# Performance work log

Hardware: AMD Instinct MI355X
Metric: run time of the kernel (lower is better)

Reference implementation:

```python
import jax, jax.numpy as jnp
import numpy as np
from bisect import bisect

# hyperparameters (from init_kwargs)
DELTA = 1e-4
GAMMA = 0.1
UTILITY_SCALE = -0.01
PRIORITY_RAIL = 0.5
LOSS_BALANCE = 1.0
ALPHA_ELU = 1.0
ENTROPY_THRESHOLDS = [0, 10, 50]
ENTROPY_LEVELS = [0.0, 0.05, 0.1, 1.0]
MASK_LEVEL = 10000.0

N = 512


def setup_inputs() -> dict:
    key = jax.random.key(0)
    k1, k2, k3, k4 = jax.random.split(key, 4)
    soft_adj = jax.random.uniform(k1, (N, N), dtype=jnp.float32)
    # original adjacency is a binary {0,1} float mask
    original_adj = (jax.random.uniform(k2, (N, N)) > 0.5).astype(jnp.float32)
    distances = jax.random.uniform(k3, (N, N), dtype=jnp.float32) * 100.0
    flow = jax.random.uniform(k4, (N, N), dtype=jnp.float32) * 10.0
    epoch = 20  # python int, selects entropy penalty level via bisect
    return {"soft_adj": soft_adj, "original_adj": original_adj,
            "distances": distances, "flow": flow, "epoch": epoch}


def _shortest_path(soft_adj, distances):
    """Soft (softmin via logsumexp) Floyd-Warshall all-pairs shortest path."""
    W = distances / (soft_adj + DELTA)          # [N, N] effective edge weights
    n = W.shape[0]
    w0 = W * (1.0 - jnp.eye(n, dtype=W.dtype))  # zero diagonal

    def step(w, k):
        # softmin(w, w[:,k,None] + w[None,k,:]) without materializing a stack
        path_through_k = w[:, k][:, None] + w[k, :][None, :]
        w_new = -GAMMA * jnp.logaddexp(-w / GAMMA, -path_through_k / GAMMA)
        return w_new, None

    w_dist, _ = jax.lax.scan(step, w0, jnp.arange(n))
    return w_dist


def reference(soft_adj, original_adj, distances, flow, epoch):
    loss_cost = jnp.sum(soft_adj * distances)

    shortest_paths = _shortest_path(soft_adj, distances)

    exp_ut_rail = jnp.exp(UTILITY_SCALE * shortest_paths * PRIORITY_RAIL)
    exp_ut_base = jnp.exp(UTILITY_SCALE * distances)
    choice_matrix = exp_ut_rail / (exp_ut_rail + exp_ut_base)
    distance_saved = distances - PRIORITY_RAIL * shortest_paths
    utility_gain = flow * choice_matrix * distance_saved
    utility_gain = jax.nn.elu(utility_gain, alpha=ALPHA_ELU) + ALPHA_ELU

    inverse_soft = jnp.eye(soft_adj.shape[0], dtype=soft_adj.dtype) - soft_adj
    entropy_loss = jnp.sum(jnp.square(soft_adj * inverse_soft))
    entropy_scale = ENTROPY_LEVELS[bisect(ENTROPY_THRESHOLDS, epoch)]

    mask_loss = jnp.sum(soft_adj * (1.0 - original_adj))

    return (loss_cost
            + LOSS_BALANCE * jnp.sum(utility_gain)
            + entropy_loss * entropy_scale
            + MASK_LEVEL * mask_loss)
```

## Files before the change

kernel.cpp:

```cpp
#include <hip/hip_runtime.h>
#include <math.h>

#define NN 512
#define KP 64
#define NPANEL 8
#define NTHR 256
#define NBLK 256
#define TRUNITS (448 * 112)

#define D_   0
#define V_   4160
#define B2_  8320
#define UB_  12672
#define SB_  17024
#define H_   21376
#define LDSN 25728

__device__ __forceinline__ float einit(const float* s, const float* dI, int i, int j) {
  float w = dI[i * NN + j] / (s[i * NN + j] + 1e-4f);
  if (i == j) w = 0.f;
  return expf(-10.f * w);
}

__global__ __launch_bounds__(NTHR) void fw_phase(
    const float* __restrict__ s, const float* __restrict__ dI,
    float* __restrict__ E, float* __restrict__ Cs, float* __restrict__ Rs,
    float* __restrict__ out, int p) {
  __shared__ __align__(16) float lds[LDSN];
  const int blk = blockIdx.x, tid = threadIdx.x;
  const int k0 = p * KP;

  if (blk >= 32) {
    const int gt = (blk - 32) * NTHR + tid;
    if (p == 0) {
      if (blk == 32 && tid == 0) out[0] = 0.f;
      if (gt < TRUNITS) {
        const int ii = gt / 112;
        const int jj = gt - ii * 112;
        const int i = ii + KP;
        const int j = (jj + 16) << 2;
        const int idx = i * NN + j;
        const float4 sv = *(const float4*)(s + idx);
        const float4 dv = *(const float4*)(dI + idx);
        float w0 = dv.x / (sv.x + 1e-4f); if (i == j + 0) w0 = 0.f;
        float w1 = dv.y / (sv.y + 1e-4f); if (i == j + 1) w1 = 0.f;
        float w2 = dv.z / (sv.z + 1e-4f); if (i == j + 2) w2 = 0.f;
        float w3 = dv.w / (sv.w + 1e-4f); if (i == j + 3) w3 = 0.f;
        *(float4*)(E + idx) = make_float4(expf(-10.f * w0), expf(-10.f * w1),
                                          expf(-10.f * w2), expf(-10.f * w3));
      }
    } else if (gt < TRUNITS) {
      const int ii = gt / 112;
      const int jj = gt - ii * 112;
      const int i = (ii < k0) ? ii : ii + KP;
      const int j = ((jj < (p << 4)) ? jj : jj + 16) << 2;
      const int idx = i * NN + j;
      const float* Cprev = Cs + (size_t)(p - 1) * (NN * KP);
      const float* Rprev = Rs + (size_t)(p - 1) * (KP * NN);
      float4 acc = *(const float4*)(E + idx);
      const float* crow = Cprev + (size_t)i * KP;
      const float* rcol = Rprev + j;
#pragma unroll 8
      for (int r = 0; r < KP; ++r) {
        const float cv = crow[r];
        const float4 rv = *(const float4*)(rcol + (size_t)r * NN);
        acc.x += cv * rv.x; acc.y += cv * rv.y;
        acc.z += cv * rv.z; acc.w += cv * rv.w;
      }
      *(float4*)(E + idx) = acc;
    }
    return;
  }

  const bool isC = (blk < 16);
  const int sb = (blk >> 1) & 7;
  const int h = blk & 1;
  const int sOff = sb * KP;
  const bool haveSl = (sb != p);
  const float* Cprev = Cs + (size_t)(p - 1) * (NN * KP);
  const float* Rprev = Rs + (size_t)(p - 1) * (KP * NN);

  if (p == 0) {
    for (int e = tid; e < 4096; e += NTHR) {
      const int a = e >> 6, b = e & 63;
      const float v = einit(s, dI, a, b);
      lds[D_ + a * 65 + b] = v;
      if (blk == 0) E[a * NN + b] = v;
    }
    if (haveSl) {
      if (isC) {
        for (int e = tid; e < 2048; e += NTHR) {
          const int a = 32 * h + (e >> 6), b = e & 63;
          const float v = einit(s, dI, sOff + a, b);
          lds[V_ + a * 65 + b] = v;
          E[(sOff + a) * NN + b] = v;
        }
      } else {
        for (int e = tid; e < 2048; e += NTHR) {
          const int m = e >> 5, j = 32 * h + (e & 31);
          const float v = einit(s, dI, m, sOff + j);
          lds[V_ + j * 65 + m] = v;
          E[m * NN + (sOff + j)] = v;
        }
      }
    }
  } else {
#pragma unroll
    for (int k = 0; k < 4; ++k) {
      const int e4 = tid + k * NTHR;
      const int a = e4 >> 4, b4 = (e4 & 15) << 2;
      *(float4*)&lds[B2_ + a * 68 + b4] =
          *(const float4*)(Cprev + (size_t)(k0 + a) * KP + b4);
      *(float4*)&lds[UB_ + a * 68 + b4] =
          *(const float4*)(Rprev + (size_t)a * NN + (k0 + b4));
      if (haveSl) {
        if (isC)
          *(float4*)&lds[SB_ + a * 68 + b4] =
              *(const float4*)(Cprev + (size_t)(sOff + a) * KP + b4);
        else
          *(float4*)&lds[SB_ + a * 68 + b4] =
              *(const float4*)(Rprev + (size_t)a * NN + (sOff + b4));
      }
    }
    __syncthreads();
    {
      const int r0 = (tid >> 4) << 2, m0 = (tid & 15) << 2;
      float acc[4][4];
#pragma unroll
      for (int i2 = 0; i2 < 4; ++i2) {
        const float4 ev = *(const float4*)(E + (size_t)(k0 + r0 + i2) * NN + (k0 + m0));
        acc[i2][0] = ev.x; acc[i2][1] = ev.y; acc[i2][2] = ev.z; acc[i2][3] = ev.w;
      }
      for (int rr = 0; rr < KP; ++rr) {
        const float4 b4 = *(const float4*)&lds[UB_ + rr * 68 + m0];
#pragma unroll
        for (int i2 = 0; i2 < 4; ++i2) {
          const float av = lds[B2_ + (r0 + i2) * 68 + rr];
          acc[i2][0] += av * b4.x; acc[i2][1] += av * b4.y;
          acc[i2][2] += av * b4.z; acc[i2][3] += av * b4.w;
        }
      }
#pragma unroll
      for (int i2 = 0; i2 < 4; ++i2)
#pragma unroll
        for (int j2 = 0; j2 < 4; ++j2)
          lds[D_ + (r0 + i2) * 65 + (m0 + j2)] = acc[i2][j2];
    }
  }
  __syncthreads();

  if (tid < 64) {
    float x[64];
    if (isC) {
#pragma unroll
      for (int a = 0; a < 64; ++a) x[a] = lds[D_ + a * 65 + tid];
    } else {
#pragma unroll
      for (int a = 0; a < 64; ++a) x[a] = lds[D_ + tid * 65 + a];
    }
#pragma unroll
    for (int m = 0; m < 64; ++m) {
      const float xm = x[m];
      lds[H_ + m * 68 + tid] = xm;
#pragma unroll
      for (int a = 0; a < 64; ++a) {
        const int sa = __builtin_amdgcn_readlane(__float_as_int(x[a]), m);
        x[a] += __int_as_float(sa) * xm;
      }
    }
  } else if (tid < 192) {
    const int tt = tid - 64;
    if (haveSl && p > 0) {
      float acc[4][4];
      if (isC) {
        const int r0 = 32 * h + ((tt >> 4) << 2);
        const int m0 = (tt & 15) << 2;
#pragma unroll
        for (int i2 = 0; i2 < 4; ++i2) {
          const float4 ev = *(const float4*)(E + (size_t)(sOff + r0 + i2) * NN + (k0 + m0));
          acc[i2][0] = ev.x; acc[i2][1] = ev.y; acc[i2][2] = ev.z; acc[i2][3] = ev.w;
        }
        for (int rr = 0; rr < KP; ++rr) {
          const float4 b4 = *(const float4*)&lds[UB_ + rr * 68 + m0];
#pragma unroll
          for (int i2 = 0; i2 < 4; ++i2) {
            const float av = lds[SB_ + (r0 + i2) * 68 + rr];
            acc[i2][0] += av * b4.x; acc[i2][1] += av * b4.y;
            acc[i2][2] += av * b4.z; acc[i2][3] += av * b4.w;
          }
        }
#pragma unroll
        for (int i2 = 0; i2 < 4; ++i2) {
          *(float4*)(E + (size_t)(sOff + r0 + i2) * NN + (k0 + m0)) =
              make_float4(acc[i2][0], acc[i2][1], acc[i2][2], acc[i2][3]);
#pragma unroll
          for (int j2 = 0; j2 < 4; ++j2)
            lds[V_ + (r0 + i2) * 65 + (m0 + j2)] = acc[i2][j2];
        }
      } else {
        const int r0 = (tt & 15) << 2;
        const int c0 = 32 * h + ((tt >> 4) << 2);
#pragma unroll
        for (int i2 = 0; i2 < 4; ++i2) {
          const float4 ev = *(const float4*)(E + (size_t)(k0 + r0 + i2) * NN + (sOff + c0));
          acc[i2][0] = ev.x; acc[i2][1] = ev.y; acc[i2][2] = ev.z; acc[i2][3] = ev.w;
        }
        for (int rr = 0; rr < KP; ++rr) {
          const float4 b4 = *(const float4*)&lds[SB_ + rr * 68 + c0];
#pragma unroll
          for (int i2 = 0; i2 < 4; ++i2) {
            const float av = lds[B2_ + (r0 + i2) * 68 + rr];
            acc[i2][0] += av * b4.x; acc[i2][1] += av * b4.y;
            acc[i2][2] += av * b4.z; acc[i2][3] += av * b4.w;
          }
        }
#pragma unroll
        for (int i2 = 0; i2 < 4; ++i2) {
          *(float4*)(E + (size_t)(k0 + r0 + i2) * NN + (sOff + c0)) =
              make_float4(acc[i2][0], acc[i2][1], acc[i2][2], acc[i2][3]);
#pragma unroll
          for (int j2 = 0; j2 < 4; ++j2)
            lds[V_ + (c0 + j2) * 65 + (r0 + i2)] = acc[i2][j2];
        }
      }
    } else if (!haveSl) {
      for (int e = tt; e < 4096; e += 128) {
        const int a = e >> 6, b = e & 63;
        lds[V_ + a * 65 + b] = isC ? lds[D_ + a * 65 + b] : lds[D_ + b * 65 + a];
      }
    }
  }
  __syncthreads();

  for (int cch = 0; cch < 4; ++cch) {
    const int mb = cch * 16;
    if (cch > 0 && tid < 128) {
      const int r = 32 * h + (tid & 31);
      const int g = tid >> 5;
      const int m0c = mb + 4 * g;
      const int vb = V_ + r * 65;
      float a0 = lds[vb + m0c + 0], a1 = lds[vb + m0c + 1];
      float a2 = lds[vb + m0c + 2], a3 = lds[vb + m0c + 3];
      for (int mp = 0; mp < mb; ++mp) {
        const float vr = lds[vb + mp];
        const float4 u4 = *(const float4*)&lds[H_ + mp * 68 + m0c];
        a0 += vr * u4.x; a1 += vr * u4.y; a2 += vr * u4.z; a3 += vr * u4.w;
      }
      lds[vb + m0c + 0] = a0; lds[vb + m0c + 1] = a1;
      lds[vb + m0c + 2] = a2; lds[vb + m0c + 3] = a3;
    }
    __syncthreads();
    if (tid < 32) {
      const int r = 32 * h + tid;
      const int vb = V_ + r * 65 + mb;
      float v[16];
#pragma unroll
      for (int u2 = 0; u2 < 16; ++u2) v[u2] = lds[vb + u2];
#pragma unroll
      for (int mp = 0; mp < 15; ++mp) {
        const float vmp = v[mp];
#pragma unroll
        for (int m2 = mp + 1; m2 < 16; ++m2)
          v[m2] += vmp * lds[H_ + (mb + mp) * 68 + (mb + m2)];
      }
#pragma unroll
      for (int u2 = 0; u2 < 16; ++u2) lds[vb + u2] = v[u2];
    }
    __syncthreads();
  }

  float* Cp = Cs + (size_t)p * (NN * KP);
  float* Rp = Rs + (size_t)p * (KP * NN);
  if (isC) {
    for (int e = tid; e < 2048; e += NTHR) {
      const int a = 32 * h + (e >> 6), b = e & 63;
      Cp[(size_t)(sOff + a) * KP + b] = lds[V_ + a * 65 + b];
    }
  } else {
    for (int e = tid; e < 2048; e += NTHR) {
      const int m = e >> 5, j = 32 * h + (e & 31);
      Rp[(size_t)m * NN + (sOff + j)] = lds[V_ + j * 65 + m];
    }
  }
}

__device__ __forceinline__ float loss_elem(float Ev, float sv, float ov,
                                           float dv, float fv, int i, int j,
                                           float esc) {
  const float sp = (Ev > 0.f) ? (-0.1f * logf(Ev)) : 1e9f;
  const float ur = expf(-0.005f * sp);
  const float ub = expf(-0.01f * dv);
  const float choice = ur / (ur + ub);
  const float ug = fv * choice * (dv - 0.5f * sp);
  const float util = (ug > 0.f) ? (ug + 1.f) : expf(ug);
  const float ent = sv * (((i == j) ? 1.f : 0.f) - sv);
  return sv * dv + util + esc * ent * ent + 10000.f * (sv * (1.f - ov));
}

__global__ __launch_bounds__(NTHR) void k_loss(
    const float* __restrict__ s, const float* __restrict__ o,
    const float* __restrict__ dI, const float* __restrict__ f,
    const int* __restrict__ ep, const float* __restrict__ E,
    const float* __restrict__ Cs, const float* __restrict__ Rs,
    float* __restrict__ out) {
  __shared__ float red[NTHR];
  const int tid = threadIdx.x;
  const int g = blockIdx.x * NTHR + tid;
  const int idx0 = g * 4;
  const int i = idx0 >> 9;
  const int j = idx0 & (NN - 1);
  const float* C7 = Cs + (size_t)7 * (NN * KP);
  const float* R7 = Rs + (size_t)7 * (KP * NN);
  float4 acc = *(const float4*)(E + idx0);
  {
    const float* crow = C7 + (size_t)i * KP;
    const float* rcol = R7 + j;
#pragma unroll 8
    for (int r = 0; r < KP; ++r) {
      const float cv = crow[r];
      const float4 rv = *(const float4*)(rcol + (size_t)r * NN);
      acc.x += cv * rv.x; acc.y += cv * rv.y;
      acc.z += cv * rv.z; acc.w += cv * rv.w;
    }
  }
  const int bi = i >> 6, bj = j >> 6;
  if (bi == bj && bi >= 1) {
    const float* cf = Cs + (size_t)(bi - 1) * (NN * KP) + (size_t)i * KP;
    const float* rf = Rs + (size_t)(bi - 1) * (KP * NN) + j;
#pragma unroll 8
    for (int r = 0; r < KP; ++r) {
      const float cv = cf[r];
      const float4 rv = *(const float4*)(rf + (size_t)r * NN);
      acc.x += cv * rv.x; acc.y += cv * rv.y;
      acc.z += cv * rv.z; acc.w += cv * rv.w;
    }
  }
  const float4 sv = *(const float4*)(s + idx0);
  const float4 ov = *(const float4*)(o + idx0);
  const float4 dv = *(const float4*)(dI + idx0);
  const float4 fv = *(const float4*)(f + idx0);
  const int e = ep[0];
  const float esc = (e < 0) ? 0.f : (e < 10) ? 0.05f : (e < 50) ? 0.1f : 1.f;
  float lsum = loss_elem(acc.x, sv.x, ov.x, dv.x, fv.x, i, j + 0, esc)
             + loss_elem(acc.y, sv.y, ov.y, dv.y, fv.y, i, j + 1, esc)
             + loss_elem(acc.z, sv.z, ov.z, dv.z, fv.z, i, j + 2, esc)
             + loss_elem(acc.w, sv.w, ov.w, dv.w, fv.w, i, j + 3, esc);
  red[tid] = lsum;
  __syncthreads();
#pragma unroll
  for (int st = 128; st > 0; st >>= 1) {
    if (tid < st) red[tid] += red[tid + st];
    __syncthreads();
  }
  if (tid == 0) atomicAdd(out, red[0]);
}

extern "C" void kernel_launch(void* const* d_in, const int* in_sizes, int n_in,
                              void* d_out, int out_size, void* d_ws, size_t ws_size,
                              hipStream_t stream) {
  const float* s = (const float*)d_in[0];
  const float* o = (const float*)d_in[1];
  const float* d = (const float*)d_in[2];
  const float* f = (const float*)d_in[3];
  const int* ep = (const int*)d_in[4];

  float* E = (float*)d_ws;
  float* Cs = E + NN * NN;
  float* Rs = Cs + NPANEL * NN * KP;
  float* out = (float*)d_out;

  for (int p = 0; p < NPANEL; ++p)
    fw_phase<<<NBLK, NTHR, 0, stream>>>(s, d, E, Cs, Rs, out, p);
  k_loss<<<NBLK, NTHR, 0, stream>>>(s, o, d, f, ep, E, Cs, Rs, out);
}
```

Measured before the change: 244.3 us.

## Overlap panel evolution with triangular solve chunks and vectorize LDS GEMM loads

```diff
diff --git a/kernel.cpp b/kernel.cpp
--- a/kernel.cpp
+++ b/kernel.cpp
@@ -20,6 +20,55 @@
   float w = dI[i * NN + j] / (s[i * NN + j] + 1e-4f);
   if (i == j) w = 0.f;
   return expf(-10.f * w);
+}
+
+template <int M0, int M1>
+__device__ __forceinline__ void evolve_seg(float* lds, float (&x)[64], int tid) {
+#pragma unroll
+  for (int m = M0; m < M1; ++m) {
+    const float xm = x[m];
+    lds[H_ + m * 68 + tid] = xm;
+#pragma unroll
+    for (int a = m + 1; a < 64; ++a) {
+      const int sa = __builtin_amdgcn_readlane(__float_as_int(x[a]), m);
+      x[a] += __int_as_float(sa) * xm;
+    }
+  }
+}
+
+__device__ __forceinline__ void pgemm_chunk(float* lds, int cch, int tt2, int h) {
+  const int mb = cch * 16;
+  const int r = 32 * h + (tt2 & 31);
+  const int g = tt2 >> 5;
+  const int m0c = mb + 4 * g;
+  const int vb = V_ + r * 65;
+  float a0 = lds[vb + m0c + 0], a1 = lds[vb + m0c + 1];
+  float a2 = lds[vb + m0c + 2], a3 = lds[vb + m0c + 3];
+  for (int mp = 0; mp < mb; ++mp) {
+    const float vr = lds[vb + mp];
+    const float4 u4 = *(const float4*)&lds[H_ + mp * 68 + m0c];
+    a0 += vr * u4.x; a1 += vr * u4.y; a2 += vr * u4.z; a3 += vr * u4.w;
+  }
+  lds[vb + m0c + 0] = a0; lds[vb + m0c + 1] = a1;
+  lds[vb + m0c + 2] = a2; lds[vb + m0c + 3] = a3;
+}
+
+__device__ __forceinline__ void micro_chunk(float* lds, int cch, int t3, int h) {
+  const int mb = cch * 16;
+  const int r = 32 * h + t3;
+  const int vb = V_ + r * 65 + mb;
+  float v[16];
+#pragma unroll
+  for (int u2 = 0; u2 < 16; ++u2) v[u2] = lds[vb + u2];
+#pragma unroll
+  for (int mp = 0; mp < 15; ++mp) {
+    const float vmp = v[mp];
+#pragma unroll
+    for (int m2 = mp + 1; m2 < 16; ++m2)
+      v[m2] += vmp * lds[H_ + (mb + mp) * 68 + (mb + m2)];
+  }
+#pragma unroll
+  for (int u2 = 0; u2 < 16; ++u2) lds[vb + u2] = v[u2];
 }
 
 __global__ __launch_bounds__(NTHR) void fw_phase(
@@ -131,13 +180,21 @@
         const float4 ev = *(const float4*)(E + (size_t)(k0 + r0 + i2) * NN + (k0 + m0));
         acc[i2][0] = ev.x; acc[i2][1] = ev.y; acc[i2][2] = ev.z; acc[i2][3] = ev.w;
       }
-      for (int rr = 0; rr < KP; ++rr) {
-        const float4 b4 = *(const float4*)&lds[UB_ + rr * 68 + m0];
-#pragma unroll
-        for (int i2 = 0; i2 < 4; ++i2) {
-          const float av = lds[B2_ + (r0 + i2) * 68 + rr];
-          acc[i2][0] += av * b4.x; acc[i2][1] += av * b4.y;
-          acc[i2][2] += av * b4.z; acc[i2][3] += av * b4.w;
+      for (int rr = 0; rr < KP; rr += 4) {
+        float4 av[4];
+#pragma unroll
+        for (int i2 = 0; i2 < 4; ++i2)
+          av[i2] = *(const float4*)&lds[B2_ + (r0 + i2) * 68 + rr];
+#pragma unroll
+        for (int k = 0; k < 4; ++k) {
+          const float4 b4 = *(const float4*)&lds[UB_ + (rr + k) * 68 + m0];
+#pragma unroll
+          for (int i2 = 0; i2 < 4; ++i2) {
+            const float a = (k == 0) ? av[i2].x : (k == 1) ? av[i2].y
+                          : (k == 2) ? av[i2].z : av[i2].w;
+            acc[i2][0] += a * b4.x; acc[i2][1] += a * b4.y;
+            acc[i2][2] += a * b4.z; acc[i2][3] += a * b4.w;
+          }
         }
       }
 #pragma unroll
@@ -149,8 +206,8 @@
   }
   __syncthreads();
 
+  float x[64];
   if (tid < 64) {
-    float x[64];
     if (isC) {
 #pragma unroll
       for (int a = 0; a < 64; ++a) x[a] = lds[D_ + a * 65 + tid];
@@ -158,16 +215,7 @@
 #pragma unroll
       for (int a = 0; a < 64; ++a) x[a] = lds[D_ + tid * 65 + a];
     }
-#pragma unroll
-    for (int m = 0; m < 64; ++m) {
-      const float xm = x[m];
-      lds[H_ + m * 68 + tid] = xm;
-#pragma unroll
-      for (int a = 0; a < 64; ++a) {
-        const int sa = __builtin_amdgcn_readlane(__float_as_int(x[a]), m);
-        x[a] += __int_as_float(sa) * xm;
-      }
-    }
+    evolve_seg<0, 16>(lds, x, tid);
   } else if (tid < 192) {
     const int tt = tid - 64;
     if (haveSl && p > 0) {
@@ -180,13 +228,21 @@
           const float4 ev = *(const float4*)(E + (size_t)(sOff + r0 + i2) * NN + (k0 + m0));
           acc[i2][0] = ev.x; acc[i2][1] = ev.y; acc[i2][2] = ev.z; acc[i2][3] = ev.w;
         }
-        for (int rr = 0; rr < KP; ++rr) {
-          const float4 b4 = *(const float4*)&lds[UB_ + rr * 68 + m0];
-#pragma unroll
-          for (int i2 = 0; i2 < 4; ++i2) {
-            const float av = lds[SB_ + (r0 + i2) * 68 + rr];
-            acc[i2][0] += av * b4.x; acc[i2][1] += av * b4.y;
-            acc[i2][2] += av * b4.z; acc[i2][3] += av * b4.w;
+        for (int rr = 0; rr < KP; rr += 4) {
+          float4 av[4];
+#pragma unroll
+          for (int i2 = 0; i2 < 4; ++i2)
+            av[i2] = *(const float4*)&lds[SB_ + (r0 + i2) * 68 + rr];
+#pragma unroll
+          for (int k = 0; k < 4; ++k) {
+            const float4 b4 = *(const float4*)&lds[UB_ + (rr + k) * 68 + m0];
+#pragma unroll
+            for (int i2 = 0; i2 < 4; ++i2) {
+              const float a = (k == 0) ? av[i2].x : (k == 1) ? av[i2].y
+                            : (k == 2) ? av[i2].z : av[i2].w;
+              acc[i2][0] += a * b4.x; acc[i2][1] += a * b4.y;
+              acc[i2][2] += a * b4.z; acc[i2][3] += a * b4.w;
+            }
           }
         }
 #pragma unroll
@@ -205,13 +261,21 @@
           const float4 ev = *(const float4*)(E + (size_t)(k0 + r0 + i2) * NN + (sOff + c0));
           acc[i2][0] = ev.x; acc[i2][1] = ev.y; acc[i2][2] = ev.z; acc[i2][3] = ev.w;
         }
-        for (int rr = 0; rr < KP; ++rr) {
-          const float4 b4 = *(const float4*)&lds[SB_ + rr * 68 + c0];
-#pragma unroll
-          for (int i2 = 0; i2 < 4; ++i2) {
-            const float av = lds[B2_ + (r0 + i2) * 68 + rr];
-            acc[i2][0] += av * b4.x; acc[i2][1] += av * b4.y;
-            acc[i2][2] += av * b4.z; acc[i2][3] += av * b4.w;
+        for (int rr = 0; rr < KP; rr += 4) {
+          float4 av[4];
+#pragma unroll
+          for (int i2 = 0; i2 < 4; ++i2)
+            av[i2] = *(const float4*)&lds[B2_ + (r0 + i2) * 68 + rr];
+#pragma unroll
+          for (int k = 0; k < 4; ++k) {
+            const float4 b4 = *(const float4*)&lds[SB_ + (rr + k) * 68 + c0];
+#pragma unroll
+            for (int i2 = 0; i2 < 4; ++i2) {
+              const float a = (k == 0) ? av[i2].x : (k == 1) ? av[i2].y
+                            : (k == 2) ? av[i2].z : av[i2].w;
+              acc[i2][0] += a * b4.x; acc[i2][1] += a * b4.y;
+              acc[i2][2] += a * b4.z; acc[i2][3] += a * b4.w;
+            }
           }
         }
 #pragma unroll
@@ -232,42 +296,26 @@
   }
   __syncthreads();
 
-  for (int cch = 0; cch < 4; ++cch) {
-    const int mb = cch * 16;
-    if (cch > 0 && tid < 128) {
-      const int r = 32 * h + (tid & 31);
-      const int g = tid >> 5;
-      const int m0c = mb + 4 * g;
-      const int vb = V_ + r * 65;
-      float a0 = lds[vb + m0c + 0], a1 = lds[vb + m0c + 1];
-      float a2 = lds[vb + m0c + 2], a3 = lds[vb + m0c + 3];
-      for (int mp = 0; mp < mb; ++mp) {
-        const float vr = lds[vb + mp];
-        const float4 u4 = *(const float4*)&lds[H_ + mp * 68 + m0c];
-        a0 += vr * u4.x; a1 += vr * u4.y; a2 += vr * u4.z; a3 += vr * u4.w;
-      }
-      lds[vb + m0c + 0] = a0; lds[vb + m0c + 1] = a1;
-      lds[vb + m0c + 2] = a2; lds[vb + m0c + 3] = a3;
-    }
-    __syncthreads();
-    if (tid < 32) {
-      const int r = 32 * h + tid;
-      const int vb = V_ + r * 65 + mb;
-      float v[16];
-#pragma unroll
-      for (int u2 = 0; u2 < 16; ++u2) v[u2] = lds[vb + u2];
-#pragma unroll
-      for (int mp = 0; mp < 15; ++mp) {
-        const float vmp = v[mp];
-#pragma unroll
-        for (int m2 = mp + 1; m2 < 16; ++m2)
-          v[m2] += vmp * lds[H_ + (mb + mp) * 68 + (mb + m2)];
-      }
-#pragma unroll
-      for (int u2 = 0; u2 < 16; ++u2) lds[vb + u2] = v[u2];
-    }
-    __syncthreads();
-  }
+  if (tid < 64) evolve_seg<16, 32>(lds, x, tid);
+  else if (tid >= 192 && tid < 224) micro_chunk(lds, 0, tid - 192, h);
+  __syncthreads();
+
+  if (tid < 64) evolve_seg<32, 48>(lds, x, tid);
+  else if (tid < 192) pgemm_chunk(lds, 1, tid - 64, h);
+  __syncthreads();
+
+  if (tid < 64) evolve_seg<48, 64>(lds, x, tid);
+  else if (tid >= 192 && tid < 224) micro_chunk(lds, 1, tid - 192, h);
+  __syncthreads();
+
+  if (tid >= 64 && tid < 192) pgemm_chunk(lds, 2, tid - 64, h);
+  __syncthreads();
+  if (tid >= 192 && tid < 224) micro_chunk(lds, 2, tid - 192, h);
+  __syncthreads();
+  if (tid >= 64 && tid < 192) pgemm_chunk(lds, 3, tid - 64, h);
+  __syncthreads();
+  if (tid >= 192 && tid < 224) micro_chunk(lds, 3, tid - 192, h);
+  __syncthreads();
 
   float* Cp = Cs + (size_t)p * (NN * KP);
   float* Rp = Rs + (size_t)p * (KP * NN);
```

Result: faster. 220.4 us (-9.8%).
